# Kernel tuning notes

Measured on AMD Instinct MI355X. Metric: run time of the kernel, lower is better.

The kernel has to match this reference:

```python
import jax, jax.numpy as jnp
import numpy as np

H = 256
V = 50257
L = 2048
B = 32


def setup_inputs() -> dict:
    key = jax.random.key(0)
    ks = jax.random.split(key, 14)
    s = 0.05  # weight scale
    return {
        "tokens": jax.random.randint(ks[0], (B,), 0, V),
        "hidden": jax.random.normal(ks[1], (1, B, H), jnp.float32),
        "cell": jax.random.normal(ks[2], (1, B, H), jnp.float32),
        "encoder_outputs": jax.random.normal(ks[3], (B, L, H), jnp.float32),
        "emb_table": jax.random.normal(ks[4], (V, H), jnp.float32) * s,
        "W_attn": jax.random.normal(ks[5], (H, 2 * H), jnp.float32) * s,
        "b_attn": jax.random.normal(ks[6], (H,), jnp.float32) * s,
        "v": jax.random.normal(ks[7], (H,), jnp.float32) * s,
        "W_ih": jax.random.normal(ks[8], (4 * H, 2 * H), jnp.float32) * s,
        "b_ih": jax.random.normal(ks[9], (4 * H,), jnp.float32) * s,
        "W_hh": jax.random.normal(ks[10], (4 * H, H), jnp.float32) * s,
        "b_hh": jax.random.normal(ks[11], (4 * H,), jnp.float32) * s,
        "W_out": jax.random.normal(ks[12], (V, 2 * H), jnp.float32) * s,
        "b_out": jax.random.normal(ks[13], (V,), jnp.float32) * s,
    }


def reference(tokens, hidden, cell, encoder_outputs, emb_table, W_attn, b_attn, v,
              W_ih, b_ih, W_hh, b_hh, W_out, b_out):
    # embedded: (B, H); dropout is identity in eval mode
    embedded = emb_table[tokens]
    h_last = hidden[-1]  # (B, H)

    # Bahdanau-style energy: attn(cat(h, e)) then dot with v (NO tanh, per source)
    # split the 2H-input linear into hidden part and encoder part
    Wh, We = W_attn[:, :H], W_attn[:, H:]
    eh = h_last @ Wh.T                                      # (B, H)
    ee = jnp.einsum('blh,kh->blk', encoder_outputs, We)     # (B, L, H)
    energy = eh[:, None, :] + ee + b_attn                   # (B, L, H)
    scores = energy @ v                                     # (B, L)
    attn_weights = jax.nn.softmax(scores, axis=-1)          # (B, L)

    # context = bmm(attn_weights, encoder_outputs)
    attn_applied = jnp.einsum('bl,blh->bh', attn_weights, encoder_outputs)  # (B, H)

    # single-step LSTM, input = cat(embedded, context): (B, 2H)
    x = jnp.concatenate([embedded, attn_applied], axis=-1)
    gates = x @ W_ih.T + b_ih + hidden[0] @ W_hh.T + b_hh   # (B, 4H)
    i_g, f_g, g_g, o_g = jnp.split(gates, 4, axis=-1)
    c_new = jax.nn.sigmoid(f_g) * cell[0] + jax.nn.sigmoid(i_g) * jnp.tanh(g_g)
    h_new = jax.nn.sigmoid(o_g) * jnp.tanh(c_new)           # (B, H)

    # output projection on cat(lstm_out, context): (B, 2H) -> (B, V)
    logits = jnp.concatenate([h_new, attn_applied], axis=-1) @ W_out.T + b_out
    log_probs = jax.nn.log_softmax(logits, axis=-1)

    return (log_probs, h_new[None], c_new[None], attn_weights[:, None, :])
```

## Files before the change

### kernel.cpp

```cpp
#include <hip/hip_runtime.h>
#include <cstddef>

#define H   256
#define L   2048
#define B   32
#define V   50257
#define H2  512
#define H4  1024

#define LP_OFF 0
#define HN_OFF (B*V)
#define CN_OFF (HN_OFF + B*H)
#define AW_OFF (CN_OFF + B*H)

#define WS_W     0
#define WS_XG    256
#define WS_XL    (WS_XG + B*H2)
#define WS_S     (WS_XL + B*H2)
#define WS_AV    (WS_S + B*L)
#define WS_AM    (WS_AV + 512*256)
#define WS_AZ    (WS_AM + 512)
#define WS_GATES (WS_AZ + 512)
#define WS_PM    (WS_GATES + B*H4)
#define WS_PZ    (WS_PM + 12800)
#define WS_M     (WS_PZ + 12800)
#define WS_LZ    (WS_M + 32)

#define NBLK_LOG 393

typedef __attribute__((ext_vector_type(8))) short bf16x8;
typedef __attribute__((ext_vector_type(4))) float f32x4;

__device__ inline unsigned short f2bf(float f) {
    unsigned u = __builtin_bit_cast(unsigned, f);
    u += 0x7FFFu + ((u >> 16) & 1u);
    return (unsigned short)(u >> 16);
}

__global__ __launch_bounds__(1024) void k_prep(const float* __restrict__ W_attn,
                                               const float* __restrict__ v,
                                               float* __restrict__ ws) {
    __shared__ float wred[1024];
    int t = threadIdx.x;
    int kq = t >> 8;
    int h  = t & 255;
    const float* base = W_attn + H + h;
    float acc = 0.f;
    #pragma unroll 16
    for (int k = kq * 64; k < kq * 64 + 64; k++) acc += v[k] * base[(size_t)k * H2];
    wred[t] = acc;
    __syncthreads();
    if (t < 256) ws[WS_W + t] = wred[t] + wred[256 + t] + wred[512 + t] + wred[768 + t];
}

__global__ __launch_bounds__(256) void k_attn_flash(const float* __restrict__ enc,
                                                    float* __restrict__ ws) {
    int bid = blockIdx.x;
    int b = bid >> 4, chunk = bid & 15;
    int t = threadIdx.x;
    int wave = t >> 6, lane = t & 63;
    __shared__ float s_lds[128];
    __shared__ float p_lds[128];
    __shared__ float red[128];
    __shared__ float vec_lds[4][256];

    const float4* w4p = (const float4*)(ws + WS_W);
    float4 wv = w4p[lane];
    size_t rowbase = (size_t)b * L + chunk * 128;

    for (int i = 0; i < 32; i++) {
        int l = wave * 32 + i;
        const float4* e4 = (const float4*)(enc + (rowbase + l) * H);
        float4 a = e4[lane];
        float p = a.x * wv.x + a.y * wv.y + a.z * wv.z + a.w * wv.w;
        #pragma unroll
        for (int off = 32; off; off >>= 1) p += __shfl_down(p, off);
        if (lane == 0) s_lds[l] = p;
    }
    __syncthreads();
    if (t < 128) { ws[WS_S + rowbase + t] = s_lds[t]; red[t] = s_lds[t]; }
    __syncthreads();
    for (int off = 64; off; off >>= 1) { if (t < off) red[t] = fmaxf(red[t], red[t + off]); __syncthreads(); }
    float m = red[0];
    __syncthreads();
    if (t < 128) { float e = __expf(s_lds[t] - m); p_lds[t] = e; red[t] = e; }
    __syncthreads();
    for (int off = 64; off; off >>= 1) { if (t < off) red[t] += red[t + off]; __syncthreads(); }

    float4 acc = make_float4(0.f, 0.f, 0.f, 0.f);
    const float4* ebase = (const float4*)(enc + (rowbase + wave * 32) * H);
    #pragma unroll 4
    for (int i = 0; i < 32; i++) {
        float p = p_lds[wave * 32 + i];
        float4 a = ebase[i * 64 + lane];
        acc.x += p * a.x; acc.y += p * a.y; acc.z += p * a.z; acc.w += p * a.w;
    }
    *(float4*)&vec_lds[wave][lane * 4] = acc;
    __syncthreads();
    ws[WS_AV + (size_t)bid * 256 + t] = vec_lds[0][t] + vec_lds[1][t] + vec_lds[2][t] + vec_lds[3][t];
    if (t == 0) { ws[WS_AM + bid] = m; ws[WS_AZ + bid] = red[0]; }
}

__global__ __launch_bounds__(256) void k_attn_comb(const int* __restrict__ tokens,
                                                   const float* __restrict__ emb,
                                                   float* __restrict__ ws,
                                                   float* __restrict__ out) {
    int b = blockIdx.x, t = threadIdx.x;
    __shared__ float mc[16], zc[16];
    if (t < 16) { mc[t] = ws[WS_AM + b * 16 + t]; zc[t] = ws[WS_AZ + b * 16 + t]; }
    __syncthreads();
    float M = -1e30f;
    #pragma unroll
    for (int c = 0; c < 16; c++) M = fmaxf(M, mc[c]);
    float Z = 0.f;
    #pragma unroll
    for (int c = 0; c < 16; c++) Z += zc[c] * __expf(mc[c] - M);
    float inv = 1.f / Z;
    float acc = 0.f;
    #pragma unroll
    for (int c = 0; c < 16; c++) acc += __expf(mc[c] - M) * ws[WS_AV + (size_t)(b * 16 + c) * 256 + t];
    acc *= inv;
    ws[WS_XG + b * H2 + H + t] = acc;
    ws[WS_XL + b * H2 + H + t] = acc;
    int tok = tokens[b];
    ws[WS_XG + b * H2 + t] = emb[(size_t)tok * H + t];
    #pragma unroll
    for (int j = 0; j < 8; j++) {
        int l = t + 256 * j;
        out[AW_OFF + (size_t)b * L + l] = __expf(ws[WS_S + (size_t)b * L + l] - M) * inv;
    }
}

__global__ __launch_bounds__(256) void k_gates(const float* __restrict__ W_ih, const float* __restrict__ b_ih,
                                               const float* __restrict__ W_hh, const float* __restrict__ b_hh,
                                               const float* __restrict__ hidden, float* __restrict__ ws) {
    int t = threadIdx.x;
    int wave = t >> 6, lane = t & 63;
    int o = blockIdx.x * 4 + wave;
    int b = o >> 10, j = o & 1023;
    const float4* wi = (const float4*)(W_ih + (size_t)j * H2);
    const float4* xg = (const float4*)(ws + WS_XG + (size_t)b * H2);
    float4 a0 = wi[lane * 2], a1 = wi[lane * 2 + 1];
    float4 x0 = xg[lane * 2], x1 = xg[lane * 2 + 1];
    float p = a0.x * x0.x + a0.y * x0.y + a0.z * x0.z + a0.w * x0.w
            + a1.x * x1.x + a1.y * x1.y + a1.z * x1.z + a1.w * x1.w;
    const float4* wh = (const float4*)(W_hh + (size_t)j * H);
    const float4* hp = (const float4*)(hidden + (size_t)b * H);
    float4 a2 = wh[lane], x2 = hp[lane];
    p += a2.x * x2.x + a2.y * x2.y + a2.z * x2.z + a2.w * x2.w;
    #pragma unroll
    for (int off = 32; off; off >>= 1) p += __shfl_down(p, off);
    if (lane == 0) ws[WS_GATES + o] = p + b_ih[j] + b_hh[j];
}

__global__ __launch_bounds__(256) void k_lstm(const float* __restrict__ cell,
                                              float* __restrict__ ws, float* __restrict__ out) {
    int b = blockIdx.x, t = threadIdx.x;
    const float* g = ws + WS_GATES + (size_t)b * H4;
    float ig = g[t], fg = g[H + t], gg = g[2 * H + t], og = g[3 * H + t];
    float c = cell[(size_t)b * H + t];
    float si = 1.f / (1.f + expf(-ig));
    float sf = 1.f / (1.f + expf(-fg));
    float so = 1.f / (1.f + expf(-og));
    float cn = sf * c + si * tanhf(gg);
    float hn = so * tanhf(cn);
    out[HN_OFF + b * H + t] = hn;
    out[CN_OFF + b * H + t] = cn;
    ws[WS_XL + b * H2 + t] = hn;
}

__global__ __launch_bounds__(256) void k_logits(const float* __restrict__ W_out,
                                                const float* __restrict__ b_out,
                                                float* __restrict__ ws,
                                                float* __restrict__ out) {
    __shared__ unsigned short Xl[32 * 520];
    int t = threadIdx.x;
    const float4* xl4 = (const float4*)(ws + WS_XL);
    #pragma unroll
    for (int it = 0; it < 16; it++) {
        int fi = t + 256 * it;
        int b = fi >> 7, kq = fi & 127;
        float4 xv = xl4[b * 128 + kq];
        unsigned p0 = (unsigned)f2bf(xv.x) | ((unsigned)f2bf(xv.y) << 16);
        unsigned p1 = (unsigned)f2bf(xv.z) | ((unsigned)f2bf(xv.w) << 16);
        unsigned* dst = (unsigned*)&Xl[b * 520 + kq * 4];
        dst[0] = p0; dst[1] = p1;
    }
    __syncthreads();

    int wave = t >> 6, lane = t & 63, quad = lane >> 4, m = lane & 15;
    int rbase = blockIdx.x * 128 + wave * 32;
    f32x4 zero4 = {0.f, 0.f, 0.f, 0.f};
    f32x4 acc[2][2];
    acc[0][0] = zero4; acc[0][1] = zero4; acc[1][0] = zero4; acc[1][1] = zero4;

    int r0 = rbase + m;
    int r1 = rbase + 16 + m;
    bool v0 = r0 < V, v1 = r1 < V;
    const float* wp0 = W_out + (size_t)r0 * H2 + quad * 8;
    const float* wp1 = W_out + (size_t)r1 * H2 + quad * 8;

    for (int kp = 0; kp < 16; kp++) {
        int k0 = kp * 32;
        bf16x8 a0 = {0,0,0,0,0,0,0,0}, a1 = {0,0,0,0,0,0,0,0};
        if (v0) {
            float4 lo = *(const float4*)(wp0 + k0);
            float4 hi = *(const float4*)(wp0 + k0 + 4);
            a0[0]=(short)f2bf(lo.x); a0[1]=(short)f2bf(lo.y); a0[2]=(short)f2bf(lo.z); a0[3]=(short)f2bf(lo.w);
            a0[4]=(short)f2bf(hi.x); a0[5]=(short)f2bf(hi.y); a0[6]=(short)f2bf(hi.z); a0[7]=(short)f2bf(hi.w);
        }
        if (v1) {
            float4 lo = *(const float4*)(wp1 + k0);
            float4 hi = *(const float4*)(wp1 + k0 + 4);
            a1[0]=(short)f2bf(lo.x); a1[1]=(short)f2bf(lo.y); a1[2]=(short)f2bf(lo.z); a1[3]=(short)f2bf(lo.w);
            a1[4]=(short)f2bf(hi.x); a1[5]=(short)f2bf(hi.y); a1[6]=(short)f2bf(hi.z); a1[7]=(short)f2bf(hi.w);
        }
        bf16x8 b0 = *(bf16x8*)&Xl[(size_t)m * 520 + k0 + quad * 8];
        bf16x8 b1 = *(bf16x8*)&Xl[(size_t)(16 + m) * 520 + k0 + quad * 8];
        acc[0][0] = __builtin_amdgcn_mfma_f32_16x16x32_bf16(a0, b0, acc[0][0], 0, 0, 0);
        acc[0][1] = __builtin_amdgcn_mfma_f32_16x16x32_bf16(a0, b1, acc[0][1], 0, 0, 0);
        acc[1][0] = __builtin_amdgcn_mfma_f32_16x16x32_bf16(a1, b0, acc[1][0], 0, 0, 0);
        acc[1][1] = __builtin_amdgcn_mfma_f32_16x16x32_bf16(a1, b1, acc[1][1], 0, 0, 0);
    }

    float val[2][2][4];
    #pragma unroll
    for (int s = 0; s < 2; s++) {
        #pragma unroll
        for (int i = 0; i < 4; i++) {
            int rr = rbase + s * 16 + quad * 4 + i;
            float bo = (rr < V) ? b_out[rr] : 0.f;
            #pragma unroll
            for (int nt = 0; nt < 2; nt++) {
                float vv = acc[s][nt][i] + bo;
                if (rr < V) {
                    int bcol = nt * 16 + m;
                    out[(size_t)bcol * V + rr] = vv;
                    val[s][nt][i] = vv;
                } else {
                    val[s][nt][i] = -1e30f;
                }
            }
        }
    }
    float pm[2], pz[2];
    #pragma unroll
    for (int nt = 0; nt < 2; nt++) {
        float mx = -1e30f;
        #pragma unroll
        for (int s = 0; s < 2; s++)
            #pragma unroll
            for (int i = 0; i < 4; i++) mx = fmaxf(mx, val[s][nt][i]);
        float sm = 0.f;
        #pragma unroll
        for (int s = 0; s < 2; s++)
            #pragma unroll
            for (int i = 0; i < 4; i++) sm += __expf(val[s][nt][i] - mx);
        pm[nt] = mx; pz[nt] = sm;
    }
    #pragma unroll
    for (int off = 16; off <= 32; off <<= 1) {
        #pragma unroll
        for (int nt = 0; nt < 2; nt++) {
            float om = __shfl_xor(pm[nt], off);
            float oz = __shfl_xor(pz[nt], off);
            float nm = fmaxf(pm[nt], om);
            pz[nt] = pz[nt] * __expf(pm[nt] - nm) + oz * __expf(om - nm);
            pm[nt] = nm;
        }
    }
    __syncthreads();
    float* red = (float*)Xl;
    if (quad == 0) {
        #pragma unroll
        for (int nt = 0; nt < 2; nt++) {
            red[wave * 32 + nt * 16 + m]       = pm[nt];
            red[128 + wave * 32 + nt * 16 + m] = pz[nt];
        }
    }
    __syncthreads();
    if (t < 32) {
        float mf = -1e30f;
        #pragma unroll
        for (int w = 0; w < 4; w++) mf = fmaxf(mf, red[w * 32 + t]);
        float z = 0.f;
        #pragma unroll
        for (int w = 0; w < 4; w++) z += red[128 + w * 32 + t] * __expf(red[w * 32 + t] - mf);
        ws[WS_PM + t * 400 + blockIdx.x] = mf;
        ws[WS_PZ + t * 400 + blockIdx.x] = z;
    }
}

__global__ __launch_bounds__(256) void k_lsm_comb(float* __restrict__ ws) {
    int b = blockIdx.x, t = threadIdx.x;
    float m = -1e30f, z = 0.f;
    for (int i = t; i < NBLK_LOG; i += 256) {
        float mi = ws[WS_PM + b * 400 + i];
        float zi = ws[WS_PZ + b * 400 + i];
        float nm = fmaxf(m, mi);
        z = z * __expf(m - nm) + zi * __expf(mi - nm);
        m = nm;
    }
    __shared__ float rm[256], rz[256];
    rm[t] = m; rz[t] = z; __syncthreads();
    for (int off = 128; off; off >>= 1) {
        if (t < off) {
            float m2 = rm[t + off], z2 = rz[t + off];
            float nm = fmaxf(rm[t], m2);
            rz[t] = rz[t] * __expf(rm[t] - nm) + z2 * __expf(m2 - nm);
            rm[t] = nm;
        }
        __syncthreads();
    }
    if (t == 0) { ws[WS_M + b] = rm[0]; ws[WS_LZ + b] = logf(rz[0]); }
}

__global__ __launch_bounds__(256) void k_lsm_final(const float* __restrict__ ws, float* __restrict__ out) {
    int b = blockIdx.y;
    int r = blockIdx.x * 256 + threadIdx.x;
    if (r < V) {
        size_t i = (size_t)b * V + r;
        out[i] = out[i] - ws[WS_M + b] - ws[WS_LZ + b];
    }
}

extern "C" void kernel_launch(void* const* d_in, const int* in_sizes, int n_in,
                              void* d_out, int out_size, void* d_ws, size_t ws_size,
                              hipStream_t stream) {
    const int*   tokens = (const int*)d_in[0];
    const float* hidden = (const float*)d_in[1];
    const float* cell   = (const float*)d_in[2];
    const float* enc    = (const float*)d_in[3];
    const float* emb    = (const float*)d_in[4];
    const float* W_attn = (const float*)d_in[5];
    const float* v      = (const float*)d_in[7];
    const float* W_ih   = (const float*)d_in[8];
    const float* b_ih   = (const float*)d_in[9];
    const float* W_hh   = (const float*)d_in[10];
    const float* b_hh   = (const float*)d_in[11];
    const float* W_out  = (const float*)d_in[12];
    const float* b_out  = (const float*)d_in[13];
    float* out = (float*)d_out;
    float* ws  = (float*)d_ws;

    k_prep<<<1, 1024, 0, stream>>>(W_attn, v, ws);
    k_attn_flash<<<B * 16, 256, 0, stream>>>(enc, ws);
    k_attn_comb<<<B, 256, 0, stream>>>(tokens, emb, ws, out);
    k_gates<<<(B * H4) / 4, 256, 0, stream>>>(W_ih, b_ih, W_hh, b_hh, hidden, ws);
    k_lstm<<<B, 256, 0, stream>>>(cell, ws, out);
    k_logits<<<NBLK_LOG, 256, 0, stream>>>(W_out, b_out, ws, out);
    k_lsm_comb<<<B, 256, 0, stream>>>(ws);
    k_lsm_final<<<dim3((V + 255) / 256, B), 256, 0, stream>>>(ws, out);
}
```

Before: 302.5 us.

## Parallelize attention prep and halve attention chunk size for more blocks

The W_attn·v precompute moves from one 1024-thread block to 32 blocks that each write partial sums, and every attention block then reduces those 32 partials into LDS. Attention chunks shrink from 128 to 64 rows, doubling the grid to 1024 blocks. The score dot product now has each quarter-wave handle a whole row with a 16-lane shuffle reduction instead of one full-wave reduction per row. The aim is more parallelism and less serial latency in the encoder pass, at the cost of redundant partial-sum reads in every block and a larger combine step.

Result: faster. 290.1 us (median of 2 runs) (-4.1%).

```diff
diff --git a/kernel.cpp b/kernel.cpp
--- a/kernel.cpp
+++ b/kernel.cpp
@@ -7,20 +7,22 @@
 #define V   50257
 #define H2  512
 #define H4  1024
+#define CH  64
+#define NCH (L/CH)
 
 #define LP_OFF 0
 #define HN_OFF (B*V)
 #define CN_OFF (HN_OFF + B*H)
 #define AW_OFF (CN_OFF + B*H)
 
-#define WS_W     0
-#define WS_XG    256
+#define WS_WP    0
+#define WS_XG    (WS_WP + 32*256)
 #define WS_XL    (WS_XG + B*H2)
 #define WS_S     (WS_XL + B*H2)
 #define WS_AV    (WS_S + B*L)
-#define WS_AM    (WS_AV + 512*256)
-#define WS_AZ    (WS_AM + 512)
-#define WS_GATES (WS_AZ + 512)
+#define WS_AM    (WS_AV + B*NCH*H)
+#define WS_AZ    (WS_AM + B*NCH)
+#define WS_GATES (WS_AZ + B*NCH)
 #define WS_PM    (WS_GATES + B*H4)
 #define WS_PZ    (WS_PM + 12800)
 #define WS_M     (WS_PZ + 12800)
@@ -37,61 +39,76 @@
     return (unsigned short)(u >> 16);
 }
 
-__global__ __launch_bounds__(1024) void k_prep(const float* __restrict__ W_attn,
-                                               const float* __restrict__ v,
-                                               float* __restrict__ ws) {
-    __shared__ float wred[1024];
-    int t = threadIdx.x;
-    int kq = t >> 8;
-    int h  = t & 255;
-    const float* base = W_attn + H + h;
+__global__ __launch_bounds__(256) void k_prep(const float* __restrict__ W_attn,
+                                              const float* __restrict__ v,
+                                              float* __restrict__ ws) {
+    int p = blockIdx.x, t = threadIdx.x;
+    const float* base = W_attn + H + t;
     float acc = 0.f;
-    #pragma unroll 16
-    for (int k = kq * 64; k < kq * 64 + 64; k++) acc += v[k] * base[(size_t)k * H2];
-    wred[t] = acc;
-    __syncthreads();
-    if (t < 256) ws[WS_W + t] = wred[t] + wred[256 + t] + wred[512 + t] + wred[768 + t];
+    #pragma unroll
+    for (int kk = 0; kk < 8; kk++) {
+        int k = p * 8 + kk;
+        acc += v[k] * base[(size_t)k * H2];
+    }
+    ws[WS_WP + p * 256 + t] = acc;
 }
 
 __global__ __launch_bounds__(256) void k_attn_flash(const float* __restrict__ enc,
                                                     float* __restrict__ ws) {
     int bid = blockIdx.x;
-    int b = bid >> 4, chunk = bid & 15;
+    int b = bid >> 5, chunk = bid & (NCH - 1);
     int t = threadIdx.x;
     int wave = t >> 6, lane = t & 63;
-    __shared__ float s_lds[128];
-    __shared__ float p_lds[128];
-    __shared__ float red[128];
+    int g = lane >> 4, u = lane & 15;
+    __shared__ float w_s[256];
+    __shared__ float s_lds[CH];
+    __shared__ float p_lds[CH];
+    __shared__ float red[CH];
     __shared__ float vec_lds[4][256];
 
-    const float4* w4p = (const float4*)(ws + WS_W);
-    float4 wv = w4p[lane];
-    size_t rowbase = (size_t)b * L + chunk * 128;
-
-    for (int i = 0; i < 32; i++) {
-        int l = wave * 32 + i;
-        const float4* e4 = (const float4*)(enc + (rowbase + l) * H);
-        float4 a = e4[lane];
-        float p = a.x * wv.x + a.y * wv.y + a.z * wv.z + a.w * wv.w;
-        #pragma unroll
-        for (int off = 32; off; off >>= 1) p += __shfl_down(p, off);
-        if (lane == 0) s_lds[l] = p;
-    }
-    __syncthreads();
-    if (t < 128) { ws[WS_S + rowbase + t] = s_lds[t]; red[t] = s_lds[t]; }
-    __syncthreads();
-    for (int off = 64; off; off >>= 1) { if (t < off) red[t] = fmaxf(red[t], red[t + off]); __syncthreads(); }
+    float wsum = 0.f;
+    #pragma unroll 8
+    for (int p = 0; p < 32; p++) wsum += ws[WS_WP + p * 256 + t];
+    w_s[t] = wsum;
+    __syncthreads();
+
+    size_t rowbase = (size_t)b * L + chunk * CH;
+    const float4* w4s = (const float4*)w_s;
+    float4 w0 = w4s[u], w1 = w4s[16 + u], w2 = w4s[32 + u], w3 = w4s[48 + u];
+
+    #pragma unroll
+    for (int ir = 0; ir < 4; ir++) {
+        int rl = wave * 16 + ir * 4 + g;
+        const float4* e4 = (const float4*)(enc + (rowbase + rl) * H);
+        float4 a0 = e4[u], a1 = e4[16 + u], a2 = e4[32 + u], a3 = e4[48 + u];
+        float p = a0.x * w0.x + a0.y * w0.y + a0.z * w0.z + a0.w * w0.w
+                + a1.x * w1.x + a1.y * w1.y + a1.z * w1.z + a1.w * w1.w
+                + a2.x * w2.x + a2.y * w2.y + a2.z * w2.z + a2.w * w2.w
+                + a3.x * w3.x + a3.y * w3.y + a3.z * w3.z + a3.w * w3.w;
+        p += __shfl_down(p, 8); p += __shfl_down(p, 4);
+        p += __shfl_down(p, 2); p += __shfl_down(p, 1);
+        if (u == 0) s_lds[rl] = p;
+    }
+    __syncthreads();
+
+    if (t < CH) red[t] = s_lds[t];
+    __syncthreads();
+    for (int off = 32; off; off >>= 1) { if (t < off) red[t] = fmaxf(red[t], red[t + off]); __syncthreads(); }
     float m = red[0];
     __syncthreads();
-    if (t < 128) { float e = __expf(s_lds[t] - m); p_lds[t] = e; red[t] = e; }
-    __syncthreads();
-    for (int off = 64; off; off >>= 1) { if (t < off) red[t] += red[t + off]; __syncthreads(); }
+    if (t < CH) {
+        float e = __expf(s_lds[t] - m);
+        p_lds[t] = e; red[t] = e;
+        ws[WS_S + rowbase + t] = s_lds[t];
+    }
+    __syncthreads();
+    for (int off = 32; off; off >>= 1) { if (t < off) red[t] += red[t + off]; __syncthreads(); }
 
     float4 acc = make_float4(0.f, 0.f, 0.f, 0.f);
-    const float4* ebase = (const float4*)(enc + (rowbase + wave * 32) * H);
+    const float4* ebase = (const float4*)(enc + (rowbase + wave * 16) * H);
     #pragma unroll 4
-    for (int i = 0; i < 32; i++) {
-        float p = p_lds[wave * 32 + i];
+    for (int i = 0; i < 16; i++) {
+        float p = p_lds[wave * 16 + i];
         float4 a = ebase[i * 64 + lane];
         acc.x += p * a.x; acc.y += p * a.y; acc.z += p * a.z; acc.w += p * a.w;
     }
@@ -106,19 +123,19 @@
                                                    float* __restrict__ ws,
                                                    float* __restrict__ out) {
     int b = blockIdx.x, t = threadIdx.x;
-    __shared__ float mc[16], zc[16];
-    if (t < 16) { mc[t] = ws[WS_AM + b * 16 + t]; zc[t] = ws[WS_AZ + b * 16 + t]; }
+    __shared__ float mc[NCH], zc[NCH];
+    if (t < NCH) { mc[t] = ws[WS_AM + b * NCH + t]; zc[t] = ws[WS_AZ + b * NCH + t]; }
     __syncthreads();
     float M = -1e30f;
     #pragma unroll
-    for (int c = 0; c < 16; c++) M = fmaxf(M, mc[c]);
+    for (int c = 0; c < NCH; c++) M = fmaxf(M, mc[c]);
     float Z = 0.f;
     #pragma unroll
-    for (int c = 0; c < 16; c++) Z += zc[c] * __expf(mc[c] - M);
+    for (int c = 0; c < NCH; c++) Z += zc[c] * __expf(mc[c] - M);
     float inv = 1.f / Z;
     float acc = 0.f;
-    #pragma unroll
-    for (int c = 0; c < 16; c++) acc += __expf(mc[c] - M) * ws[WS_AV + (size_t)(b * 16 + c) * 256 + t];
+    #pragma unroll 8
+    for (int c = 0; c < NCH; c++) acc += __expf(mc[c] - M) * ws[WS_AV + (size_t)(b * NCH + c) * 256 + t];
     acc *= inv;
     ws[WS_XG + b * H2 + H + t] = acc;
     ws[WS_XL + b * H2 + H + t] = acc;
@@ -343,8 +360,8 @@
     float* out = (float*)d_out;
     float* ws  = (float*)d_ws;
 
-    k_prep<<<1, 1024, 0, stream>>>(W_attn, v, ws);
-    k_attn_flash<<<B * 16, 256, 0, stream>>>(enc, ws);
+    k_prep<<<32, 256, 0, stream>>>(W_attn, v, ws);
+    k_attn_flash<<<B * NCH, 256, 0, stream>>>(enc, ws);
     k_attn_comb<<<B, 256, 0, stream>>>(tokens, emb, ws, out);
     k_gates<<<(B * H4) / 4, 256, 0, stream>>>(W_ih, b_ih, W_hh, b_hh, hidden, ws);
     k_lstm<<<B, 256, 0, stream>>>(cell, ws, out);
```
